# Kernel optimization log

Measured on AMD Instinct MI355X. Metric: run time of the kernel, lower is better.

The kernel has to match this reference:

```python
import jax, jax.numpy as jnp
import numpy as np

D_LATENT = 128   # per-head dim AND input embedding dim (d_q default)
N_HEADS = 16
ROPE_BASE = 10000.0


def _rope(x):
    # x: [B, H, S, D]; interleaved-pair rotary embedding over seq axis (-2)
    B, H, S, D = x.shape
    half = D // 2
    inv_freq = 1.0 / (ROPE_BASE ** (jnp.arange(half, dtype=jnp.float32) * 2.0 / D))
    ang = jnp.arange(S, dtype=jnp.float32)[:, None] * inv_freq[None, :]  # [S, half]
    cos, sin = jnp.cos(ang), jnp.sin(ang)
    xp = x.reshape(B, H, S, half, 2)
    x0, x1 = xp[..., 0], xp[..., 1]
    r0 = x0 * cos - x1 * sin
    r1 = x1 * cos + x0 * sin
    return jnp.stack([r0, r1], axis=-1).reshape(B, H, S, D)


def setup_inputs() -> dict:
    key = jax.random.key(0)
    k_q, k_wq, k_wk, k_wv, k_wo = jax.random.split(key, 5)
    B, S, E = 2, 2048, D_LATENT
    inner = N_HEADS * D_LATENT
    sc_in = 1.0 / np.sqrt(E)
    sc_inner = 1.0 / np.sqrt(inner)
    return {
        "q": jax.random.normal(k_q, (B, S, E), dtype=jnp.float32),
        "W_q": jax.random.normal(k_wq, (E, inner), dtype=jnp.float32) * sc_in,
        "W_k": jax.random.normal(k_wk, (E, inner), dtype=jnp.float32) * sc_in,
        "W_v": jax.random.normal(k_wv, (E, inner), dtype=jnp.float32) * sc_in,
        "W_o": jax.random.normal(k_wo, (inner, E), dtype=jnp.float32) * sc_inner,
    }


def reference(q, W_q, W_k, W_v, W_o):
    B, S, E = q.shape
    H, D = N_HEADS, D_LATENT
    scale = 1.0 / np.sqrt(D)
    # projections -> [B, H, S, D]
    qh = (q @ W_q).reshape(B, S, H, D).transpose(0, 2, 1, 3)
    kh = (q @ W_k).reshape(B, S, H, D).transpose(0, 2, 1, 3)
    vh = (q @ W_v).reshape(B, S, H, D).transpose(0, 2, 1, 3)
    qh = _rope(qh)
    kh = _rope(kh)
    scores = jnp.einsum("bhsd,bhtd->bhst", qh, kh) * scale  # [B,H,S,S]
    causal = jnp.tril(jnp.ones((S, S), dtype=bool))
    scores = jnp.where(causal, scores, -jnp.inf)
    probs = jax.nn.softmax(scores, axis=-1)
    out = jnp.einsum("bhst,bhtd->bhsd", probs, vh)  # [B,H,S,D]
    out = out.transpose(0, 2, 1, 3).reshape(B, S, H * D)
    return out @ W_o
```

## Files before the change

### kernel.cpp

```cpp
#include <hip/hip_runtime.h>
#include <math.h>

#define S_LEN 2048
#define NH 16
#define DH 128
#define INNER 2048
#define NROWS 4096

typedef __attribute__((ext_vector_type(8))) short bf16x8;
typedef __attribute__((ext_vector_type(4))) float f32x4;
typedef __attribute__((ext_vector_type(2))) unsigned int u32x2;

__device__ __forceinline__ short f2bf(float f) {
  union { float f; unsigned u; } v; v.f = f;
  unsigned r = (v.u + 0x7fffu + ((v.u >> 16) & 1u)) >> 16;
  return (short)(unsigned short)r;
}
__device__ __forceinline__ float bf2f(short s) {
  union { unsigned u; float f; } v; v.u = ((unsigned)(unsigned short)s) << 16;
  return v.f;
}
__device__ __forceinline__ int pkbf(float lo, float hi) {
  union { float f; unsigned u; } x, y;
  x.f = lo; y.f = hi;
  return (int)__builtin_amdgcn_perm(y.u + 0x8000u, x.u + 0x8000u, 0x07060302u);
}
__device__ __forceinline__ void gl2lds(const short* g, short* l) {
  __builtin_amdgcn_global_load_lds(
      (const __attribute__((address_space(1))) unsigned int*)g,
      (__attribute__((address_space(3))) unsigned int*)l, 16, 0, 0);
}
__device__ __forceinline__ void pl32swap(int& a, int& b) {
  u32x2 r = __builtin_amdgcn_permlane32_swap((unsigned)a, (unsigned)b, false, false);
  a = (int)r.x; b = (int)r.y;
}
__device__ __forceinline__ void pl16swap(int& a, int& b) {
  u32x2 r = __builtin_amdgcn_permlane16_swap((unsigned)a, (unsigned)b, false, false);
  a = (int)r.x; b = (int)r.y;
}

__global__ void k_prep(const float* __restrict__ X, const float* __restrict__ Wq,
                       const float* __restrict__ Wk, const float* __restrict__ Wv,
                       const float* __restrict__ Wo,
                       float* __restrict__ csT, short* __restrict__ Xbf,
                       short* __restrict__ WT, short* __restrict__ WoT,
                       float* __restrict__ outz) {
  const int bx = blockIdx.x, tid = threadIdx.x;
  if (bx < 512) {
    int idx = bx * 256 + tid;
    int i = idx & 63, s = idx >> 6;
    double invf = pow(10000.0, -(double)i / 64.0);
    float ang = (float)((double)s * invf);
    float sv, cv; sincosf(ang, &sv, &cv);
    csT[idx * 2] = cv; csT[idx * 2 + 1] = sv;
    return;
  }
  if (bx < 1024) {
    int idx = ((bx - 512) * 256 + tid) * 4;
    float4 xv = *(const float4*)&X[idx];
    short4 o; o.x = f2bf(xv.x); o.y = f2bf(xv.y); o.z = f2bf(xv.z); o.w = f2bf(xv.w);
    *(short4*)&Xbf[idx] = o;
    return;
  }
  if (bx >= 2048) {
    float4 z4 = make_float4(0.f, 0.f, 0.f, 0.f);
    ((float4*)outz)[(bx - 2048) * 512 + tid] = z4;
    ((float4*)outz)[(bx - 2048) * 512 + tid + 256] = z4;
    return;
  }
  __shared__ float tile[32][33];
  const float* src; short* dst; int R, C, c0, r0;
  if (bx < 1792) {
    int z = (bx - 1024) >> 8, t = (bx - 1024) & 255;
    src = (z == 0) ? Wq : ((z == 1) ? Wk : Wv);
    dst = WT + (size_t)z * INNER * 128; R = 128; C = INNER;
    c0 = (t & 63) * 32; r0 = (t >> 6) * 32;
  } else {
    int t = bx - 1792;
    src = Wo; dst = WoT; R = INNER; C = 128;
    c0 = (t & 3) * 32; r0 = (t >> 2) * 32;
  }
  int tx = tid & 31, ty = tid >> 5;
  #pragma unroll
  for (int dy = 0; dy < 32; dy += 8)
    tile[ty + dy][tx] = src[(size_t)(r0 + ty + dy) * C + c0 + tx];
  __syncthreads();
  #pragma unroll
  for (int dy = 0; dy < 32; dy += 8)
    dst[(size_t)(c0 + ty + dy) * R + r0 + tx] = f2bf(tile[tx][ty + dy]);
}

__global__ __launch_bounds__(256, 2) void k_qkv(
    const short* __restrict__ Xbf, const short* __restrict__ WT,
    const float* __restrict__ csT,
    short* __restrict__ Qg, short* __restrict__ Kg, short* __restrict__ Vg) {
  __shared__ __attribute__((aligned(16))) short As[128 * 136];
  __shared__ __attribute__((aligned(16))) short Bs[128 * 136];
  const int tid = threadIdx.x;
  const int n0 = blockIdx.x * 128, m0 = blockIdx.y * 128;
  for (int e = tid; e < 2048; e += 256)
    *(int4*)&As[(e >> 4) * 136 + (e & 15) * 8] =
        *(const int4*)&Xbf[(size_t)(m0 + (e >> 4)) * 128 + (e & 15) * 8];
  const int wid = tid >> 6, lane = tid & 63;
  const int l16 = lane & 15, quad = lane >> 4;
  const int wm = (wid & 1) * 64, wn = (wid >> 1) * 64;
  const int hh = n0 >> 7;
  const int bb = m0 >> 11, ss = m0 & 2047;
  const float qscale = 0.12751745f;
  for (int z = 0; z < 3; ++z) {
    __syncthreads();
    const short* Wp = WT + (size_t)z * INNER * 128;
    for (int e = tid; e < 2048; e += 256)
      *(int4*)&Bs[(e >> 4) * 136 + (e & 15) * 8] =
          *(const int4*)&Wp[(size_t)(n0 + (e >> 4)) * 128 + (e & 15) * 8];
    __syncthreads();
    f32x4 acc[4][4] = {};
    #pragma unroll
    for (int ks = 0; ks < 4; ++ks) {
      bf16x8 ax[4], bw[4];
      #pragma unroll
      for (int j = 0; j < 4; ++j) {
        ax[j] = *(const bf16x8*)&As[(wm + j * 16 + l16) * 136 + ks * 32 + quad * 8];
        bw[j] = *(const bf16x8*)&Bs[(wn + j * 16 + l16) * 136 + ks * 32 + quad * 8];
      }
      if (z < 2) {
        #pragma unroll
        for (int dt = 0; dt < 4; ++dt)
          #pragma unroll
          for (int st = 0; st < 4; ++st)
            acc[dt][st] = __builtin_amdgcn_mfma_f32_16x16x32_bf16(bw[dt], ax[st], acc[dt][st], 0, 0, 0);
      } else {
        #pragma unroll
        for (int mt = 0; mt < 4; ++mt)
          #pragma unroll
          for (int nt = 0; nt < 4; ++nt)
            acc[mt][nt] = __builtin_amdgcn_mfma_f32_16x16x32_bf16(ax[mt], bw[nt], acc[mt][nt], 0, 0, 0);
      }
    }
    if (z < 2) {
      __syncthreads();
      #pragma unroll
      for (int dt = 0; dt < 4; ++dt)
        #pragma unroll
        for (int st = 0; st < 4; ++st) {
          int d0 = wn + dt * 16 + quad * 4;
          int sl = wm + st * 16 + l16;
          int sg = ss + sl;
          float4 cs = *(const float4*)&csT[((size_t)sg * 64 + (d0 >> 1)) * 2];
          float x0 = acc[dt][st][0], x1 = acc[dt][st][1];
          float x2 = acc[dt][st][2], x3 = acc[dt][st][3];
          float r0 = x0 * cs.x - x1 * cs.y, r1 = x1 * cs.x + x0 * cs.y;
          float r2 = x2 * cs.z - x3 * cs.w, r3 = x3 * cs.z + x2 * cs.w;
          if (z == 0) { r0 *= qscale; r1 *= qscale; r2 *= qscale; r3 *= qscale; }
          int2 pk; pk.x = pkbf(r0, r1); pk.y = pkbf(r2, r3);
          *(int2*)&Bs[sl * 136 + d0] = pk;
        }
      __syncthreads();
      short* dst = (z == 0 ? Qg : Kg) + (((size_t)(bb * NH + hh)) * S_LEN + ss) * DH;
      #pragma unroll
      for (int it = 0; it < 8; ++it) {
        int u = tid + 256 * it;
        int row = u >> 4, c = u & 15;
        int cc = (z == 0) ? c : (c ^ (row & 15));
        *(int4*)&dst[(size_t)row * DH + cc * 8] = *(const int4*)&Bs[row * 136 + c * 8];
      }
    } else {
      __syncthreads();
      #pragma unroll
      for (int mt = 0; mt < 4; ++mt)
        #pragma unroll
        for (int nt = 0; nt < 4; ++nt) {
          int dl = wn + nt * 16 + l16;
          int sl = wm + mt * 16 + quad * 4;
          int2 pk;
          pk.x = pkbf(acc[mt][nt][0], acc[mt][nt][1]);
          pk.y = pkbf(acc[mt][nt][2], acc[mt][nt][3]);
          *(int2*)&As[dl * 136 + sl] = pk;
        }
      __syncthreads();
      #pragma unroll
      for (int rd = 0; rd < 8; ++rd) {
        int dl = (tid >> 4) + rd * 16;
        int sl = (tid & 15) * 8;
        int tile = (ss >> 6) + (sl >> 6);
        int tl = sl & 63;
        int ch = (tl >> 3) ^ (dl & 7);
        int4 vv = *(const int4*)&As[dl * 136 + sl];
        *(int4*)&Vg[(((size_t)(bb * NH + hh) * 32 + tile) * 128 + dl) * 64 + ch * 8] = vv;
      }
    }
  }
}

__global__ __launch_bounds__(256, 2) void k_attn(
    const short* __restrict__ Qg, const short* __restrict__ Kg,
    const short* __restrict__ Vt, short* __restrict__ Op,
    float* __restrict__ mlb) {
  __shared__ __attribute__((aligned(16))) short Ks[2][64 * 128];
  __shared__ __attribute__((aligned(16))) short Vs[2][128 * 64];
  const int bid = blockIdx.x;
  const int bh = bid & 31, unit = bid >> 5;
  const int tid = threadIdx.x, wid = tid >> 6, lane = tid & 63;
  const int l16 = lane & 15, quad = lane >> 4, wq = wid * 32;
  const float CEXP2 = 23.083121f;
  const short* Qp = Qg + (size_t)bh * S_LEN * DH;
  const short* Kp = Kg + (size_t)bh * S_LEN * DH;
  const short* Vb = Vt + (size_t)bh * 32 * 8192;
  int kcs[4], vcs[2];
  #pragma unroll
  for (int ks = 0; ks < 4; ++ks) kcs[ks] = ((ks * 4 + quad) ^ l16) * 8;
  #pragma unroll
  for (int ks = 0; ks < 2; ++ks) vcs[ks] = ((ks * 4 + quad) ^ (l16 & 7)) * 8;

  for (int seg = 0; seg < 2; ++seg) {
    const int qg = seg ? (15 - unit) : unit;
    const int par = seg;
    const int q0 = qg * 128, nj = qg + 1;
    __syncthreads();
    {
      const short* kg = Kp + (size_t)(par * 64) * DH;
      const short* vg = Vb + (size_t)par * 8192;
      #pragma unroll
      for (int i = 0; i < 4; ++i) {
        int sl = wid * 4 + i;
        gl2lds(kg + sl * 512 + lane * 8, &Ks[0][sl * 512]);
        gl2lds(vg + sl * 512 + lane * 8, &Vs[0][sl * 512]);
      }
    }
    bf16x8 qf[4][2];
    #pragma unroll
    for (int ks = 0; ks < 4; ++ks)
      #pragma unroll
      for (int qb = 0; qb < 2; ++qb)
        qf[ks][qb] = *(const bf16x8*)&Qp[(size_t)(q0 + wq + qb * 16 + l16) * DH +
                                         ks * 32 + quad * 8];
    float l_p[2] = {0.0f, 0.0f};
    f32x4 Oacc[8][2] = {};
    for (int jj = 0; jj < nj; ++jj) {
      const int b = jj & 1;
      const int j = par + 2 * jj;
      __syncthreads();
      if (jj + 1 < nj) {
        const int jn = par + 2 * (jj + 1);
        const short* kg = Kp + (size_t)(jn * 64) * DH;
        const short* vg = Vb + (size_t)jn * 8192;
        #pragma unroll
        for (int i = 0; i < 4; ++i) {
          int sl = wid * 4 + i;
          gl2lds(kg + sl * 512 + lane * 8, &Ks[1 - b][sl * 512]);
          gl2lds(vg + sl * 512 + lane * 8, &Vs[1 - b][sl * 512]);
        }
      }
      f32x4 Sc[4][2] = {};
      #pragma unroll
      for (int ks = 0; ks < 4; ++ks) {
        bf16x8 kfr[4];
        #pragma unroll
        for (int nt = 0; nt < 4; ++nt)
          kfr[nt] = *(const bf16x8*)&Ks[b][(nt * 16 + l16) * 128 + kcs[ks]];
        __builtin_amdgcn_s_setprio(1);
        #pragma unroll
        for (int nt = 0; nt < 4; ++nt)
          #pragma unroll
          for (int qb = 0; qb < 2; ++qb)
            Sc[nt][qb] = __builtin_amdgcn_mfma_f32_16x16x32_bf16(kfr[nt], qf[ks][qb],
                                                                 Sc[nt][qb], 0, 0, 0);
        __builtin_amdgcn_s_setprio(0);
      }
      if (jj == nj - 1) {
        #pragma unroll
        for (int nt = 0; nt < 4; ++nt)
          #pragma unroll
          for (int qb = 0; qb < 2; ++qb)
            #pragma unroll
            for (int r = 0; r < 4; ++r) {
              int tg = j * 64 + nt * 16 + quad * 4 + r;
              int qgl = q0 + wq + qb * 16 + l16;
              if (tg > qgl) Sc[nt][qb][r] = -1000.0f;
            }
      }
      bf16x8 bpf[2][2];
      #pragma unroll
      for (int qb = 0; qb < 2; ++qb) {
        float ls0 = 0.0f, ls1 = 0.0f;
        #pragma unroll
        for (int nt = 0; nt < 4; ++nt)
          #pragma unroll
          for (int r = 0; r < 4; ++r) {
            float pe = __builtin_amdgcn_exp2f(Sc[nt][qb][r] - CEXP2);
            Sc[nt][qb][r] = pe;
            if (nt & 1) ls1 += pe; else ls0 += pe;
          }
        l_p[qb] += ls0 + ls1;
        int px[4], py[4];
        #pragma unroll
        for (int nt = 0; nt < 4; ++nt) {
          px[nt] = pkbf(Sc[nt][qb][0], Sc[nt][qb][1]);
          py[nt] = pkbf(Sc[nt][qb][2], Sc[nt][qb][3]);
        }
        pl32swap(px[0], px[1]); pl16swap(px[0], px[1]);
        pl32swap(py[0], py[1]); pl16swap(py[0], py[1]);
        pl32swap(px[2], px[3]); pl16swap(px[2], px[3]);
        pl32swap(py[2], py[3]); pl16swap(py[2], py[3]);
        union { int i[4]; bf16x8 v; } u0, u1;
        u0.i[0] = px[0]; u0.i[1] = py[0]; u0.i[2] = px[1]; u0.i[3] = py[1];
        u1.i[0] = px[2]; u1.i[1] = py[2]; u1.i[2] = px[3]; u1.i[3] = py[3];
        bpf[qb][0] = u0.v; bpf[qb][1] = u1.v;
      }
      #pragma unroll
      for (int ks = 0; ks < 2; ++ks) {
        bf16x8 vfr[8];
        #pragma unroll
        for (int nt = 0; nt < 8; ++nt)
          vfr[nt] = *(const bf16x8*)&Vs[b][(nt * 16 + l16) * 64 + vcs[ks]];
        __builtin_amdgcn_s_setprio(1);
        #pragma unroll
        for (int nt = 0; nt < 8; ++nt)
          #pragma unroll
          for (int qb = 0; qb < 2; ++qb)
            Oacc[nt][qb] = __builtin_amdgcn_mfma_f32_16x16x32_bf16(vfr[nt], bpf[qb][ks],
                                                                   Oacc[nt][qb], 0, 0, 0);
        __builtin_amdgcn_s_setprio(0);
      }
    }
    __syncthreads();
    short* osl = &Ks[0][0] + wid * 4096;
    #pragma unroll
    for (int qb = 0; qb < 2; ++qb)
      #pragma unroll
      for (int nt = 0; nt < 8; ++nt) {
        int2 ov;
        ov.x = pkbf(Oacc[nt][qb][0], Oacc[nt][qb][1]);
        ov.y = pkbf(Oacc[nt][qb][2], Oacc[nt][qb][3]);
        int ch = ((nt * 2 + (quad >> 1)) ^ l16) * 8 + (quad & 1) * 4;
        *(int2*)&osl[(qb * 16 + l16) * 128 + ch] = ov;
      }
    size_t obase = ((size_t)(par * 32 + bh) * S_LEN + q0 + wq) * DH;
    #pragma unroll
    for (int it = 0; it < 8; ++it) {
      int u = lane + 64 * it;
      int row = u >> 4, c = u & 15;
      *(int4*)&Op[obase + (size_t)row * DH + c * 8] =
          *(const int4*)&osl[row * 128 + ((c ^ (row & 15)) * 8)];
    }
    #pragma unroll
    for (int qb = 0; qb < 2; ++qb) {
      float lt = l_p[qb];
      lt += __shfl_xor(lt, 16);
      lt += __shfl_xor(lt, 32);
      int qrow = q0 + wq + qb * 16 + l16;
      if (quad == 0)
        mlb[(size_t)(par * 32 + bh) * S_LEN + qrow] = lt;
    }
  }
}

__global__ __launch_bounds__(256, 2) void k_out(
    const short* __restrict__ Op, const float* __restrict__ mlb,
    const short* __restrict__ WoT, float* __restrict__ out) {
  __shared__ __attribute__((aligned(16))) short As[32 * 136];
  __shared__ __attribute__((aligned(16))) short Bs[128 * 136];
  __shared__ float cw[4][32];
  const int m0 = blockIdx.x * 32, h0 = blockIdx.y * 4;
  const int tid = threadIdx.x, wid = tid >> 6, lane = tid & 63;
  const int l16 = lane & 15, quad = lane >> 4;
  const int wm = (wid & 1) * 16, wn = (wid >> 1) * 64;
  if (tid < 128) {
    int rr = tid & 31, hh = tid >> 5;
    int row = m0 + rr, b = row >> 11, s = row & 2047;
    int bh = b * NH + h0 + hh;
    float l1 = mlb[(size_t)bh * S_LEN + s];
    float l2 = mlb[(size_t)(32 + bh) * S_LEN + s];
    cw[hh][rr] = 1.0f / (l1 + l2);
  }
  __syncthreads();
  f32x4 acc[4] = {};
  for (int hc = 0; hc < 4; ++hc) {
    int h = h0 + hc;
    #pragma unroll
    for (int it = 0; it < 4; ++it) {
      int e = tid + 256 * it;
      int rr = e >> 5, c4 = (e & 31) * 4;
      int row = m0 + rr, b = row >> 11, s = row & 2047;
      size_t base = ((size_t)(b * NH + h) * S_LEN + s) * DH + c4;
      short4 u1 = *(const short4*)&Op[base];
      short4 u2 = *(const short4*)&Op[(size_t)32 * S_LEN * DH + base];
      float c1 = cw[hc][rr];
      int2 o;
      o.x = pkbf(c1 * (bf2f(u1.x) + bf2f(u2.x)), c1 * (bf2f(u1.y) + bf2f(u2.y)));
      o.y = pkbf(c1 * (bf2f(u1.z) + bf2f(u2.z)), c1 * (bf2f(u1.w) + bf2f(u2.w)));
      *(int2*)&As[rr * 136 + c4] = o;
    }
    for (int e = tid; e < 2048; e += 256)
      *(int4*)&Bs[(e >> 4) * 136 + (e & 15) * 8] =
          *(const int4*)&WoT[(size_t)(e >> 4) * INNER + h * 128 + (e & 15) * 8];
    __syncthreads();
    #pragma unroll
    for (int ks = 0; ks < 4; ++ks) {
      bf16x8 a = *(const bf16x8*)&As[(wm + l16) * 136 + ks * 32 + quad * 8];
      bf16x8 b[4];
      #pragma unroll
      for (int nt = 0; nt < 4; ++nt)
        b[nt] = *(const bf16x8*)&Bs[(wn + nt * 16 + l16) * 136 + ks * 32 + quad * 8];
      #pragma unroll
      for (int nt = 0; nt < 4; ++nt)
        acc[nt] = __builtin_amdgcn_mfma_f32_16x16x32_bf16(a, b[nt], acc[nt], 0, 0, 0);
    }
    __syncthreads();
  }
  #pragma unroll
  for (int nt = 0; nt < 4; ++nt)
    #pragma unroll
    for (int r = 0; r < 4; ++r) {
      int gm = m0 + wm + quad * 4 + r;
      int gn = wn + nt * 16 + l16;
      atomicAdd(&out[(size_t)gm * 128 + gn], acc[nt][r]);
    }
}

extern "C" void kernel_launch(void* const* d_in, const int* in_sizes, int n_in,
                              void* d_out, int out_size, void* d_ws, size_t ws_size,
                              hipStream_t stream) {
  const float* q  = (const float*)d_in[0];
  const float* Wq = (const float*)d_in[1];
  const float* Wk = (const float*)d_in[2];
  const float* Wv = (const float*)d_in[3];
  const float* Wo = (const float*)d_in[4];
  float* out = (float*)d_out;
  char* ws = (char*)d_ws;
  const size_t MB = 1024 * 1024;
  float* csT = (float*)(ws + 0);
  short* WT  = (short*)(ws + 1 * MB);
  short* WoT = (short*)(ws + 2 * MB + 512 * 1024);
  short* Xbf = (short*)(ws + 3 * MB);
  short* Qg  = (short*)(ws + 8 * MB);
  short* Kg  = (short*)(ws + 24 * MB);
  short* Vg  = (short*)(ws + 40 * MB);
  short* Op  = (short*)(ws + 56 * MB);
  float* mlb = (float*)(ws + 88 * MB);

  k_prep<<<2304, 256, 0, stream>>>(q, Wq, Wk, Wv, Wo, csT, Xbf, WT, WoT, out);
  k_qkv<<<dim3(16, 32), 256, 0, stream>>>(Xbf, WT, csT, Qg, Kg, Vg);
  k_attn<<<512, 256, 0, stream>>>(Qg, Kg, Vg, Op, mlb);
  k_out<<<dim3(128, 4), 256, 0, stream>>>(Op, mlb, WoT, out);
}
```

Measured before the change: 151.9 us.

## Share K/V tiles across two query tiles per 512-thread attention block

The attention kernel now runs 8 waves per block in two groups, each handling one adjacent 128-row query tile. Both groups consume the same double-buffered K/V tiles in LDS, so each K/V load serves twice the queries. This replaces the old scheme where one block walked two query tiles one after another. Groups with fewer causal key tiles idle through the extra iterations while still joining the barriers. The RoPE frequency computation in the prep kernel also switches from double-precision pow to a float exp2, which may slightly change the rounding of the angles.

```diff
diff --git a/kernel.cpp b/kernel.cpp
--- a/kernel.cpp
+++ b/kernel.cpp
@@ -49,8 +49,8 @@
   if (bx < 512) {
     int idx = bx * 256 + tid;
     int i = idx & 63, s = idx >> 6;
-    double invf = pow(10000.0, -(double)i / 64.0);
-    float ang = (float)((double)s * invf);
+    float invf = __builtin_amdgcn_exp2f((float)i * -0.20762051f);
+    float ang = (float)s * invf;
     float sv, cv; sincosf(ang, &sv, &cv);
     csT[idx * 2] = cv; csT[idx * 2 + 1] = sv;
     return;
@@ -192,16 +192,21 @@
   }
 }
 
-__global__ __launch_bounds__(256, 2) void k_attn(
+__global__ __launch_bounds__(512, 4) void k_attn(
     const short* __restrict__ Qg, const short* __restrict__ Kg,
     const short* __restrict__ Vt, short* __restrict__ Op,
     float* __restrict__ mlb) {
-  __shared__ __attribute__((aligned(16))) short Ks[2][64 * 128];
-  __shared__ __attribute__((aligned(16))) short Vs[2][128 * 64];
+  __shared__ __attribute__((aligned(16))) short S[4][64 * 128];
   const int bid = blockIdx.x;
-  const int bh = bid & 31, unit = bid >> 5;
+  const int half = bid >> 8, g = (bid >> 6) & 3;
+  const int bh = (bid >> 1) & 31, par = bid & 1;
+  const int u = half ? g : 7 - g;
   const int tid = threadIdx.x, wid = tid >> 6, lane = tid & 63;
-  const int l16 = lane & 15, quad = lane >> 4, wq = wid * 32;
+  const int grp = wid >> 2, wg = wid & 3;
+  const int l16 = lane & 15, quad = lane >> 4, wq = wg * 32;
+  const int qt = 2 * u + grp;
+  const int q0 = qt << 7, nj = qt + 1;
+  const int njmax = 2 * u + 2;
   const float CEXP2 = 23.083121f;
   const short* Qp = Qg + (size_t)bh * S_LEN * DH;
   const short* Kp = Kg + (size_t)bh * S_LEN * DH;
@@ -212,146 +217,141 @@
   #pragma unroll
   for (int ks = 0; ks < 2; ++ks) vcs[ks] = ((ks * 4 + quad) ^ (l16 & 7)) * 8;
 
-  for (int seg = 0; seg < 2; ++seg) {
-    const int qg = seg ? (15 - unit) : unit;
-    const int par = seg;
-    const int q0 = qg * 128, nj = qg + 1;
+  {
+    const short* kg = Kp + (size_t)(par * 64) * DH;
+    const short* vg = Vb + (size_t)par * 8192;
+    #pragma unroll
+    for (int i = 0; i < 2; ++i) {
+      int sl = wid * 2 + i;
+      gl2lds(kg + sl * 512 + lane * 8, &S[0][sl * 512]);
+      gl2lds(vg + sl * 512 + lane * 8, &S[2][sl * 512]);
+    }
+  }
+  bf16x8 qf[4][2];
+  #pragma unroll
+  for (int ks = 0; ks < 4; ++ks)
+    #pragma unroll
+    for (int qb = 0; qb < 2; ++qb)
+      qf[ks][qb] = *(const bf16x8*)&Qp[(size_t)(q0 + wq + qb * 16 + l16) * DH +
+                                       ks * 32 + quad * 8];
+  float l_p[2] = {0.0f, 0.0f};
+  f32x4 Oacc[8][2] = {};
+  for (int jj = 0; jj < njmax; ++jj) {
+    const int b = jj & 1;
+    const int j = par + 2 * jj;
     __syncthreads();
-    {
-      const short* kg = Kp + (size_t)(par * 64) * DH;
-      const short* vg = Vb + (size_t)par * 8192;
-      #pragma unroll
-      for (int i = 0; i < 4; ++i) {
-        int sl = wid * 4 + i;
-        gl2lds(kg + sl * 512 + lane * 8, &Ks[0][sl * 512]);
-        gl2lds(vg + sl * 512 + lane * 8, &Vs[0][sl * 512]);
-      }
-    }
-    bf16x8 qf[4][2];
-    #pragma unroll
-    for (int ks = 0; ks < 4; ++ks)
-      #pragma unroll
-      for (int qb = 0; qb < 2; ++qb)
-        qf[ks][qb] = *(const bf16x8*)&Qp[(size_t)(q0 + wq + qb * 16 + l16) * DH +
-                                         ks * 32 + quad * 8];
-    float l_p[2] = {0.0f, 0.0f};
-    f32x4 Oacc[8][2] = {};
-    for (int jj = 0; jj < nj; ++jj) {
-      const int b = jj & 1;
-      const int j = par + 2 * jj;
-      __syncthreads();
-      if (jj + 1 < nj) {
-        const int jn = par + 2 * (jj + 1);
-        const short* kg = Kp + (size_t)(jn * 64) * DH;
-        const short* vg = Vb + (size_t)jn * 8192;
-        #pragma unroll
-        for (int i = 0; i < 4; ++i) {
-          int sl = wid * 4 + i;
-          gl2lds(kg + sl * 512 + lane * 8, &Ks[1 - b][sl * 512]);
-          gl2lds(vg + sl * 512 + lane * 8, &Vs[1 - b][sl * 512]);
-        }
-      }
-      f32x4 Sc[4][2] = {};
-      #pragma unroll
-      for (int ks = 0; ks < 4; ++ks) {
-        bf16x8 kfr[4];
-        #pragma unroll
-        for (int nt = 0; nt < 4; ++nt)
-          kfr[nt] = *(const bf16x8*)&Ks[b][(nt * 16 + l16) * 128 + kcs[ks]];
-        __builtin_amdgcn_s_setprio(1);
-        #pragma unroll
-        for (int nt = 0; nt < 4; ++nt)
-          #pragma unroll
-          for (int qb = 0; qb < 2; ++qb)
-            Sc[nt][qb] = __builtin_amdgcn_mfma_f32_16x16x32_bf16(kfr[nt], qf[ks][qb],
-                                                                 Sc[nt][qb], 0, 0, 0);
-        __builtin_amdgcn_s_setprio(0);
-      }
-      if (jj == nj - 1) {
-        #pragma unroll
-        for (int nt = 0; nt < 4; ++nt)
-          #pragma unroll
-          for (int qb = 0; qb < 2; ++qb)
-            #pragma unroll
-            for (int r = 0; r < 4; ++r) {
-              int tg = j * 64 + nt * 16 + quad * 4 + r;
-              int qgl = q0 + wq + qb * 16 + l16;
-              if (tg > qgl) Sc[nt][qb][r] = -1000.0f;
-            }
-      }
-      bf16x8 bpf[2][2];
-      #pragma unroll
-      for (int qb = 0; qb < 2; ++qb) {
-        float ls0 = 0.0f, ls1 = 0.0f;
-        #pragma unroll
-        for (int nt = 0; nt < 4; ++nt)
+    if (jj + 1 < njmax) {
+      const int jn = par + 2 * (jj + 1);
+      const short* kg = Kp + (size_t)(jn * 64) * DH;
+      const short* vg = Vb + (size_t)jn * 8192;
+      #pragma unroll
+      for (int i = 0; i < 2; ++i) {
+        int sl = wid * 2 + i;
+        gl2lds(kg + sl * 512 + lane * 8, &S[1 - b][sl * 512]);
+        gl2lds(vg + sl * 512 + lane * 8, &S[3 - b][sl * 512]);
+      }
+    }
+    if (jj >= nj) continue;
+    f32x4 Sc[4][2] = {};
+    #pragma unroll
+    for (int ks = 0; ks < 4; ++ks) {
+      bf16x8 kfr[4];
+      #pragma unroll
+      for (int nt = 0; nt < 4; ++nt)
+        kfr[nt] = *(const bf16x8*)&S[b][(nt * 16 + l16) * 128 + kcs[ks]];
+      __builtin_amdgcn_s_setprio(1);
+      #pragma unroll
+      for (int nt = 0; nt < 4; ++nt)
+        #pragma unroll
+        for (int qb = 0; qb < 2; ++qb)
+          Sc[nt][qb] = __builtin_amdgcn_mfma_f32_16x16x32_bf16(kfr[nt], qf[ks][qb],
+                                                               Sc[nt][qb], 0, 0, 0);
+      __builtin_amdgcn_s_setprio(0);
+    }
+    if (jj == nj - 1) {
+      #pragma unroll
+      for (int nt = 0; nt < 4; ++nt)
+        #pragma unroll
+        for (int qb = 0; qb < 2; ++qb)
           #pragma unroll
           for (int r = 0; r < 4; ++r) {
-            float pe = __builtin_amdgcn_exp2f(Sc[nt][qb][r] - CEXP2);
-            Sc[nt][qb][r] = pe;
-            if (nt & 1) ls1 += pe; else ls0 += pe;
+            int tg = j * 64 + nt * 16 + quad * 4 + r;
+            int qgl = q0 + wq + qb * 16 + l16;
+            if (tg > qgl) Sc[nt][qb][r] = -1000.0f;
           }
-        l_p[qb] += ls0 + ls1;
-        int px[4], py[4];
-        #pragma unroll
-        for (int nt = 0; nt < 4; ++nt) {
-          px[nt] = pkbf(Sc[nt][qb][0], Sc[nt][qb][1]);
-          py[nt] = pkbf(Sc[nt][qb][2], Sc[nt][qb][3]);
+    }
+    bf16x8 bpf[2][2];
+    #pragma unroll
+    for (int qb = 0; qb < 2; ++qb) {
+      float ls0 = 0.0f, ls1 = 0.0f;
+      #pragma unroll
+      for (int nt = 0; nt < 4; ++nt)
+        #pragma unroll
+        for (int r = 0; r < 4; ++r) {
+          float pe = __builtin_amdgcn_exp2f(Sc[nt][qb][r] - CEXP2);
+          Sc[nt][qb][r] = pe;
+          if (nt & 1) ls1 += pe; else ls0 += pe;
         }
-        pl32swap(px[0], px[1]); pl16swap(px[0], px[1]);
-        pl32swap(py[0], py[1]); pl16swap(py[0], py[1]);
-        pl32swap(px[2], px[3]); pl16swap(px[2], px[3]);
-        pl32swap(py[2], py[3]); pl16swap(py[2], py[3]);
-        union { int i[4]; bf16x8 v; } u0, u1;
-        u0.i[0] = px[0]; u0.i[1] = py[0]; u0.i[2] = px[1]; u0.i[3] = py[1];
-        u1.i[0] = px[2]; u1.i[1] = py[2]; u1.i[2] = px[3]; u1.i[3] = py[3];
-        bpf[qb][0] = u0.v; bpf[qb][1] = u1.v;
-      }
-      #pragma unroll
-      for (int ks = 0; ks < 2; ++ks) {
-        bf16x8 vfr[8];
-        #pragma unroll
-        for (int nt = 0; nt < 8; ++nt)
-          vfr[nt] = *(const bf16x8*)&Vs[b][(nt * 16 + l16) * 64 + vcs[ks]];
-        __builtin_amdgcn_s_setprio(1);
-        #pragma unroll
-        for (int nt = 0; nt < 8; ++nt)
-          #pragma unroll
-          for (int qb = 0; qb < 2; ++qb)
-            Oacc[nt][qb] = __builtin_amdgcn_mfma_f32_16x16x32_bf16(vfr[nt], bpf[qb][ks],
-                                                                   Oacc[nt][qb], 0, 0, 0);
-        __builtin_amdgcn_s_setprio(0);
-      }
-    }
-    __syncthreads();
-    short* osl = &Ks[0][0] + wid * 4096;
-    #pragma unroll
-    for (int qb = 0; qb < 2; ++qb)
-      #pragma unroll
-      for (int nt = 0; nt < 8; ++nt) {
-        int2 ov;
-        ov.x = pkbf(Oacc[nt][qb][0], Oacc[nt][qb][1]);
-        ov.y = pkbf(Oacc[nt][qb][2], Oacc[nt][qb][3]);
-        int ch = ((nt * 2 + (quad >> 1)) ^ l16) * 8 + (quad & 1) * 4;
-        *(int2*)&osl[(qb * 16 + l16) * 128 + ch] = ov;
-      }
-    size_t obase = ((size_t)(par * 32 + bh) * S_LEN + q0 + wq) * DH;
-    #pragma unroll
-    for (int it = 0; it < 8; ++it) {
-      int u = lane + 64 * it;
-      int row = u >> 4, c = u & 15;
-      *(int4*)&Op[obase + (size_t)row * DH + c * 8] =
-          *(const int4*)&osl[row * 128 + ((c ^ (row & 15)) * 8)];
-    }
-    #pragma unroll
-    for (int qb = 0; qb < 2; ++qb) {
-      float lt = l_p[qb];
-      lt += __shfl_xor(lt, 16);
-      lt += __shfl_xor(lt, 32);
-      int qrow = q0 + wq + qb * 16 + l16;
-      if (quad == 0)
-        mlb[(size_t)(par * 32 + bh) * S_LEN + qrow] = lt;
-    }
+      l_p[qb] += ls0 + ls1;
+      int px[4], py[4];
+      #pragma unroll
+      for (int nt = 0; nt < 4; ++nt) {
+        px[nt] = pkbf(Sc[nt][qb][0], Sc[nt][qb][1]);
+        py[nt] = pkbf(Sc[nt][qb][2], Sc[nt][qb][3]);
+      }
+      pl32swap(px[0], px[1]); pl16swap(px[0], px[1]);
+      pl32swap(py[0], py[1]); pl16swap(py[0], py[1]);
+      pl32swap(px[2], px[3]); pl16swap(px[2], px[3]);
+      pl32swap(py[2], py[3]); pl16swap(py[2], py[3]);
+      union { int i[4]; bf16x8 v; } u0, u1;
+      u0.i[0] = px[0]; u0.i[1] = py[0]; u0.i[2] = px[1]; u0.i[3] = py[1];
+      u1.i[0] = px[2]; u1.i[1] = py[2]; u1.i[2] = px[3]; u1.i[3] = py[3];
+      bpf[qb][0] = u0.v; bpf[qb][1] = u1.v;
+    }
+    #pragma unroll
+    for (int ks = 0; ks < 2; ++ks) {
+      bf16x8 vfr[8];
+      #pragma unroll
+      for (int nt = 0; nt < 8; ++nt)
+        vfr[nt] = *(const bf16x8*)&S[2 + b][(nt * 16 + l16) * 64 + vcs[ks]];
+      __builtin_amdgcn_s_setprio(1);
+      #pragma unroll
+      for (int nt = 0; nt < 8; ++nt)
+        #pragma unroll
+        for (int qb = 0; qb < 2; ++qb)
+          Oacc[nt][qb] = __builtin_amdgcn_mfma_f32_16x16x32_bf16(vfr[nt], bpf[qb][ks],
+                                                                 Oacc[nt][qb], 0, 0, 0);
+      __builtin_amdgcn_s_setprio(0);
+    }
+  }
+  __syncthreads();
+  short* osl = &S[0][0] + wid * 4096;
+  #pragma unroll
+  for (int qb = 0; qb < 2; ++qb)
+    #pragma unroll
+    for (int nt = 0; nt < 8; ++nt) {
+      int2 ov;
+      ov.x = pkbf(Oacc[nt][qb][0], Oacc[nt][qb][1]);
+      ov.y = pkbf(Oacc[nt][qb][2], Oacc[nt][qb][3]);
+      int ch = ((nt * 2 + (quad >> 1)) ^ l16) * 8 + (quad & 1) * 4;
+      *(int2*)&osl[(qb * 16 + l16) * 128 + ch] = ov;
+    }
+  size_t obase = ((size_t)(par * 32 + bh) * S_LEN + q0 + wq) * DH;
+  #pragma unroll
+  for (int it = 0; it < 8; ++it) {
+    int u2 = lane + 64 * it;
+    int row = u2 >> 4, c = u2 & 15;
+    *(int4*)&Op[obase + (size_t)row * DH + c * 8] =
+        *(const int4*)&osl[row * 128 + ((c ^ (row & 15)) * 8)];
+  }
+  #pragma unroll
+  for (int qb = 0; qb < 2; ++qb) {
+    float lt = l_p[qb];
+    lt += __shfl_xor(lt, 16);
+    lt += __shfl_xor(lt, 32);
+    int qrow = q0 + wq + qb * 16 + l16;
+    if (quad == 0)
+      mlb[(size_t)(par * 32 + bh) * S_LEN + qrow] = lt;
   }
 }
 
@@ -441,6 +441,6 @@
 
   k_prep<<<2304, 256, 0, stream>>>(q, Wq, Wk, Wv, Wo, csT, Xbf, WT, WoT, out);
   k_qkv<<<dim3(16, 32), 256, 0, stream>>>(Xbf, WT, csT, Qg, Kg, Vg);
-  k_attn<<<512, 256, 0, stream>>>(Qg, Kg, Vg, Op, mlb);
+  k_attn<<<512, 512, 0, stream>>>(Qg, Kg, Vg, Op, mlb);
   k_out<<<dim3(128, 4), 256, 0, stream>>>(Op, mlb, WoT, out);
 }
```

Result: slower. 250.1 us (+64.6%).
